# Kernel optimization log

Hardware: AMD Instinct MI355X
Metric: run time of the kernel (lower is better)

Reference implementation:

```python
import jax, jax.numpy as jnp
import numpy as np


def setup_inputs() -> dict:
    key = jax.random.key(0)
    k1, k2, k3, k4 = jax.random.split(key, 4)
    B, Tv, Ta, D = 8, 2048, 2048, 256
    return {
        "visual_features": jax.random.normal(k1, (B, Tv, D), dtype=jnp.float32),
        "audio_features": jax.random.normal(k2, (B, Ta, D), dtype=jnp.float32),
        "visual_weights": jax.random.uniform(k3, (D, D), dtype=jnp.float32),
        "audio_weights": jax.random.uniform(k4, (D, D), dtype=jnp.float32),
        "num_neighbors": 8,
    }


def _pairwise_l2(vm, am):
    # ||v - a|| via the expanded form to avoid the [B,Tv,Ta,D] intermediate.
    sq = (
        jnp.sum(vm * vm, -1)[:, :, None]
        + jnp.sum(am * am, -1)[:, None, :]
        - 2.0 * jnp.einsum("btd,bsd->bts", vm, am)
    )
    sq = jnp.maximum(sq, 0.0)
    # safe sqrt: subgradient 0 at 0 (matches torch.norm backward convention)
    return jnp.where(sq > 0, jnp.sqrt(jnp.where(sq > 0, sq, 1.0)), 0.0)


def reference(visual_features, audio_features, visual_weights, audio_weights, num_neighbors):
    vm = visual_features @ visual_weights  # [B,Tv,D]
    am = audio_features @ audio_weights    # [B,Ta,D]
    graph = jnp.exp(-_pairwise_l2(vm, am))  # [B,Tv,Ta]
    # topk over the visual axis (dim=1): move it last for lax.top_k
    _, idx = jax.lax.top_k(jnp.swapaxes(graph, 1, 2), num_neighbors)  # [B,Ta,k]
    idx = jnp.swapaxes(idx, 1, 2)  # [B,k,Ta]
    # broadcasted gather along axis 1: result [B,k,Ta,D]
    vn = jnp.take_along_axis(visual_features[:, :, None, :], idx[..., None], axis=1)
    an = jnp.take_along_axis(audio_features[:, :, None, :], idx[..., None], axis=1)
    # mean over dim=2 (the Ta axis of the gathered neighbors) -> [B,k,D]
    return vn.mean(axis=2), an.mean(axis=2)
```

## Files before the change

### kernel.cpp

```cpp
#include <hip/hip_runtime.h>
#include <cstddef>
#include <cstdint>

namespace {
constexpr int kB   = 8;
constexpr int kT   = 2048;
constexpr int kD   = 256;
constexpr int kK   = 8;
constexpr int kM   = kB * kT;
constexpr int kNC  = kB * kT;
constexpr int kColCap = 64;
constexpr int kOvCap  = 1 << 17;
constexpr int kStr = 264;
constexpr float kMinNormalF = 1.17549435e-38f;
}

typedef __attribute__((ext_vector_type(8)))  __bf16 bf16x8;
typedef __attribute__((ext_vector_type(16))) float  f32x16;

__device__ inline unsigned short f2bf_rne(float x) {
  unsigned u = __float_as_uint(x);
  unsigned r = (u + 0x7FFFu + ((u >> 16) & 1u)) >> 16;
  return (unsigned short)r;
}
__device__ inline float bf2f(unsigned short h) {
  return __uint_as_float((unsigned)h << 16);
}
union FragU { uint4 u4; bf16x8 v; };

__device__ inline void async16(const unsigned short* g, unsigned short* l) {
  __builtin_amdgcn_global_load_lds(
      (const __attribute__((address_space(1))) unsigned int*)(const void*)g,
      (__attribute__((address_space(3))) unsigned int*)(void*)l, 16, 0, 0);
}

__device__ inline void stage_tile_async(const unsigned short* src,
                                        unsigned short* S, int w, int lane) {
  const int hi = lane >> 5, lo = lane & 31;
#pragma unroll
  for (int i = 0; i < 8; ++i) {
    const int p = w * 8 + i;
    const int rowl = p * 2 + hi;
    const int c = lo ^ (rowl & 31);
    async16(src + (size_t)rowl * kD + c * 8, S + p * 512);
  }
}
__device__ inline uint4 lds_frag(const unsigned short* S, int row, int kc, int half) {
  const int c = (kc * 2 + half) ^ (row & 31);
  return *reinterpret_cast<const uint4*>(S + row * 256 + c * 8);
}

__global__ __launch_bounds__(256) void prep(const float* __restrict__ W0,
                                            const float* __restrict__ W1,
                                            unsigned short* __restrict__ T0,
                                            unsigned short* __restrict__ T1,
                                            unsigned* __restrict__ zeroBase,
                                            int zeroWords) {
  const int blk = blockIdx.x;
  if (blk < 128) {
    const float* W = (blk & 64) ? W1 : W0;
    unsigned short* WT = (blk & 64) ? T1 : T0;
    const int t = blk & 63;
    const int c0 = (t & 7) * 32, k0 = (t >> 3) * 32;
    __shared__ float tile[32][33];
    const int tx = threadIdx.x & 31, ty = threadIdx.x >> 5;
#pragma unroll
    for (int i = 0; i < 4; ++i)
      tile[ty + i * 8][tx] = W[(size_t)(k0 + ty + i * 8) * kD + c0 + tx];
    __syncthreads();
#pragma unroll
    for (int i = 0; i < 4; ++i)
      WT[(size_t)(c0 + ty + i * 8) * kD + k0 + tx] = f2bf_rne(tile[tx][ty + i * 8]);
  } else {
    for (int i = (blk - 128) * 256 + threadIdx.x; i < zeroWords; i += 32 * 256)
      zeroBase[i] = 0u;
  }
}

__global__ __launch_bounds__(256) void gemm_hyb(const float* __restrict__ Xv,
                                                const float* __restrict__ Xa,
                                                const unsigned short* __restrict__ WvT,
                                                const unsigned short* __restrict__ WaT,
                                                unsigned short* __restrict__ Cv,
                                                unsigned short* __restrict__ Ca,
                                                float* __restrict__ nv,
                                                float* __restrict__ na) {
  __shared__ unsigned short S[64 * kStr];
  const int z = blockIdx.z;
  const float* X = z ? Xa : Xv;
  const unsigned short* WT = z ? WaT : WvT;
  unsigned short* Cb = z ? Ca : Cv;
  float* nrm = z ? na : nv;
  const int r0 = blockIdx.x * 64;
  const int cHalf = blockIdx.y;
  const int tid = threadIdx.x;
  const int w = tid >> 6, lane = tid & 63;
  const int wt = w & 1, wc = w >> 1;
  const int half = lane >> 5, ln = lane & 31;

#pragma unroll
  for (int i = 0; i < 16; ++i) {
    const int idx = i * 256 + tid;
    const int row = idx >> 6, g = idx & 63;
    const float4 v = *reinterpret_cast<const float4*>(X + (size_t)(r0 + row) * kD + g * 4);
    ushort4 o;
    o.x = f2bf_rne(v.x); o.y = f2bf_rne(v.y); o.z = f2bf_rne(v.z); o.w = f2bf_rne(v.w);
    *reinterpret_cast<ushort4*>(S + row * kStr + g * 4) = o;
  }
  __syncthreads();
  uint4 afr[16];
#pragma unroll
  for (int kc = 0; kc < 16; ++kc)
    afr[kc] = *reinterpret_cast<const uint4*>(S + (wt * 32 + ln) * kStr + kc * 16 + half * 8);

  float ns[16];
#pragma unroll
  for (int r = 0; r < 16; ++r) ns[r] = 0.0f;

  for (int ct = 0; ct < 2; ++ct) {
    const int c0 = (cHalf * 2 + ct) * 64;
    __syncthreads();
    stage_tile_async(WT + (size_t)c0 * kD, S, w, lane);
    __syncthreads();
    f32x16 acc;
#pragma unroll
    for (int i = 0; i < 16; ++i) acc[i] = 0.0f;
#pragma unroll
    for (int kc = 0; kc < 16; ++kc) {
      FragU fa, fb;
      fa.u4 = afr[kc];
      fb.u4 = lds_frag(S, wc * 32 + ln, kc, half);
      acc = __builtin_amdgcn_mfma_f32_32x32x16_bf16(fa.v, fb.v, acc, 0, 0, 0);
    }
    const int col = c0 + wc * 32 + ln;
#pragma unroll
    for (int r = 0; r < 16; ++r) {
      const int row = r0 + wt * 32 + (r & 3) + 8 * (r >> 2) + 4 * half;
      const unsigned short us = f2bf_rne(acc[r]);
      Cb[(size_t)row * kD + col] = us;
      const float f = bf2f(us);
      ns[r] += f * f;
    }
  }
#pragma unroll
  for (int r = 0; r < 16; ++r) {
    float v = ns[r];
#pragma unroll
    for (int off = 1; off < 32; off <<= 1) v += __shfl_xor(v, off, 64);
    if (ln == 0) {
      const int row = r0 + wt * 32 + (r & 3) + 8 * (r >> 2) + 4 * half;
      atomicAdd(nrm + row, v);
    }
  }
}

__global__ __launch_bounds__(256) void keys_v14(const unsigned short* __restrict__ vmb,
                                                const unsigned short* __restrict__ amb,
                                                const float* __restrict__ vn2,
                                                const float* __restrict__ an2,
                                                unsigned* __restrict__ colCount,
                                                uint2* __restrict__ colRecs,
                                                unsigned* __restrict__ ovCount,
                                                uint2* __restrict__ ovRecs) {
  __shared__ unsigned short S[64 * 256];
  const int b = blockIdx.z;
  const int t0 = blockIdx.x * 128;
  const int sr0 = blockIdx.y * 256;
  const int tid = threadIdx.x;
  const int w = tid >> 6, lane = tid & 63;
  const int half = lane >> 5, ln = lane & 31;

  uint4 afr[16];
#pragma unroll
  for (int h = 0; h < 2; ++h) {
    __syncthreads();
    stage_tile_async(vmb + ((size_t)b * kT + t0 + h * 64) * kD, S, w, lane);
    __syncthreads();
    if ((w >> 1) == h) {
#pragma unroll
      for (int kc = 0; kc < 16; ++kc)
        afr[kc] = lds_frag(S, (w & 1) * 32 + ln, kc, half);
    }
  }

  const float* v2p = vn2 + (size_t)b * kT + t0 + w * 32;

  for (int st = 0; st < 4; ++st) {
    const int s0 = sr0 + st * 64;
    __syncthreads();
    stage_tile_async(amb + ((size_t)b * kT + s0) * kD, S, w, lane);
    __syncthreads();
    f32x16 acc[2];
#pragma unroll
    for (int j = 0; j < 2; ++j)
#pragma unroll
      for (int i = 0; i < 16; ++i) acc[j][i] = 0.0f;
#pragma unroll
    for (int kc = 0; kc < 16; ++kc) {
      FragU fa; fa.u4 = afr[kc];
#pragma unroll
      for (int ss = 0; ss < 2; ++ss) {
        FragU fb;
        fb.u4 = lds_frag(S, ss * 32 + ln, kc, half);
        acc[ss] = __builtin_amdgcn_mfma_f32_32x32x16_bf16(fa.v, fb.v, acc[ss], 0, 0, 0);
      }
    }
#pragma unroll
    for (int ss = 0; ss < 2; ++ss) {
      const int s = s0 + ss * 32 + ln;
      const float a2 = an2[(size_t)b * kT + s];
      const int c = (b << 11) | s;
#pragma unroll
      for (int g = 0; g < 4; ++g) {
        const float4 v2 = *reinterpret_cast<const float4*>(v2p + g * 8 + half * 4);
        const float v2a[4] = {v2.x, v2.y, v2.z, v2.w};
#pragma unroll
        for (int q = 0; q < 4; ++q) {
          const float raw = v2a[q] + a2 - 2.0f * acc[ss][4 * g + q];
          if (raw < 7744.0f) {
            const float dist = sqrtf(fmaxf(raw, 0.0f));
            const float e = expf(-dist);
            if (e >= kMinNormalF) {
              const int t = t0 + w * 32 + g * 8 + half * 4 + q;
              const unsigned slot = atomicAdd(&colCount[c], 1u);
              if (slot < (unsigned)kColCap) {
                colRecs[(size_t)c * kColCap + slot] = make_uint2(__float_as_uint(e), (unsigned)t);
              } else {
                const unsigned pos = ((unsigned)b << 22) | ((unsigned)s << 11) | (unsigned)t;
                const unsigned oi = atomicAdd(ovCount, 1u);
                if (oi < (unsigned)kOvCap) ovRecs[oi] = make_uint2(__float_as_uint(e), pos);
              }
            }
          }
        }
      }
    }
  }
}

__global__ __launch_bounds__(256) void gather_fused(const float* __restrict__ visual,
                                                    const float* __restrict__ audio,
                                                    const unsigned* __restrict__ colCount,
                                                    const uint2* __restrict__ colRecs,
                                                    const unsigned* __restrict__ ovCount,
                                                    const uint2* __restrict__ ovRecs,
                                                    float* __restrict__ pv,
                                                    float* __restrict__ pa) {
  __shared__ int sIdx[32];
  const int u = blockIdx.x;
  const int bj = u >> 6, ch = u & 63;
  const int b = bj >> 3, j = bj & 7;
  const int tid = threadIdx.x;
  if (tid < 32) {
    const int s = ch * 32 + tid;
    const int c = (b << 11) | s;
    unsigned K[8]; int T[8];
#pragma unroll
    for (int i = 0; i < 8; ++i) { K[i] = 0u; T[i] = 0x7FFFFFFF; }
    const int cnt = (int)colCount[c];
    const int m = min(cnt, kColCap);
    for (int i = 0; i < m; ++i) {
      const uint2 r = colRecs[(size_t)c * kColCap + i];
      const unsigned kx = r.x; const int tx = (int)r.y;
      if (kx > K[7] || (kx == K[7] && tx < T[7])) {
        K[7] = kx; T[7] = tx;
#pragma unroll
        for (int q = 7; q >= 1; --q) {
          const bool sw = (K[q] > K[q - 1]) || (K[q] == K[q - 1] && T[q] < T[q - 1]);
          if (sw) {
            const unsigned tk = K[q]; K[q] = K[q - 1]; K[q - 1] = tk;
            const int tt = T[q];      T[q] = T[q - 1]; T[q - 1] = tt;
          }
        }
      }
    }
    if (cnt > kColCap) {
      int n = (int)*ovCount;
      if (n > kOvCap) n = kOvCap;
      for (int i = 0; i < n; ++i) {
        const uint2 r = ovRecs[i];
        if ((int)(r.y >> 11) == c) {
          const unsigned kx = r.x; const int tx = (int)(r.y & 2047u);
          if (kx > K[7] || (kx == K[7] && tx < T[7])) {
            K[7] = kx; T[7] = tx;
#pragma unroll
            for (int q = 7; q >= 1; --q) {
              const bool sw = (K[q] > K[q - 1]) || (K[q] == K[q - 1] && T[q] < T[q - 1]);
              if (sw) {
                const unsigned tk = K[q]; K[q] = K[q - 1]; K[q - 1] = tk;
                const int tt = T[q];      T[q] = T[q - 1]; T[q - 1] = tt;
              }
            }
          }
        }
      }
    }
    int mcnt = 0;
#pragma unroll
    for (int i = 0; i < 8; ++i) if (K[i] > 0u) mcnt++;
    int outv[8];
#pragma unroll
    for (int i = 0; i < 8; ++i) outv[i] = T[i];
    int cand = 0;
    for (int r = mcnt; r < 8; ++r) {
      bool taken = true;
      while (taken) {
        taken = false;
#pragma unroll
        for (int q = 0; q < 8; ++q)
          if (q < mcnt && T[q] == cand) taken = true;
        if (taken) cand++;
      }
      outv[r] = cand++;
    }
    sIdx[tid] = outv[j];
  }
  __syncthreads();
  float accV = 0.f, accA = 0.f;
  for (int i = 0; i < 32; ++i) {
    const int t = sIdx[i];
    const size_t base = ((size_t)b * kT + t) * kD + tid;
    accV += visual[base];
    accA += audio[base];
  }
  pv[(size_t)u * kD + tid] = accV;
  pa[(size_t)u * kD + tid] = accA;
}

__global__ __launch_bounds__(256) void reduce_kernel(const float* __restrict__ pv,
                                                     const float* __restrict__ pa,
                                                     float* __restrict__ out) {
  const int bj = blockIdx.x;
  const int d = threadIdx.x;
  float sV = 0.f, sA = 0.f;
#pragma unroll 8
  for (int ch = 0; ch < 64; ++ch) {
    sV += pv[((size_t)bj * 64 + ch) * kD + d];
    sA += pa[((size_t)bj * 64 + ch) * kD + d];
  }
  out[(size_t)bj * kD + d] = sV * (1.0f / kT);
  out[(size_t)kB * kK * kD + (size_t)bj * kD + d] = sA * (1.0f / kT);
}

extern "C" void kernel_launch(void* const* d_in, const int* in_sizes, int n_in,
                              void* d_out, int out_size, void* d_ws, size_t ws_size,
                              hipStream_t stream) {
  (void)in_sizes; (void)n_in; (void)out_size; (void)ws_size;
  const float* visual = (const float*)d_in[0];
  const float* audio  = (const float*)d_in[1];
  const float* Wv     = (const float*)d_in[2];
  const float* Wa     = (const float*)d_in[3];
  float* out = (float*)d_out;

  char* ws = (char*)d_ws;
  unsigned short* WvT = (unsigned short*)ws;
  unsigned short* WaT = WvT + (size_t)kD * kD;
  unsigned short* vmb = WaT + (size_t)kD * kD;
  unsigned short* amb = vmb + (size_t)kM * kD;
  float* vn2 = (float*)(amb + (size_t)kM * kD);
  float* an2 = vn2 + kM;
  unsigned* colCount = (unsigned*)(an2 + kM);
  unsigned* ovCount  = colCount + kNC;
  uint2* colRecs = (uint2*)(ovCount + 8);
  uint2* ovRecs  = colRecs + (size_t)kNC * kColCap;
  float* pv = (float*)(ovRecs + kOvCap);
  float* pa = pv + (size_t)4096 * kD;
  const int zeroWords = 2 * kM + kNC + 8;

  prep<<<dim3(160), 256, 0, stream>>>(Wv, Wa, WvT, WaT, (unsigned*)vn2, zeroWords);
  gemm_hyb<<<dim3(kM / 64, 2, 2), 256, 0, stream>>>(visual, audio, WvT, WaT,
                                                    vmb, amb, vn2, an2);
  keys_v14<<<dim3(kT / 128, kT / 256, kB), 256, 0, stream>>>(vmb, amb, vn2, an2,
                                                             colCount, colRecs, ovCount, ovRecs);
  gather_fused<<<dim3(4096), 256, 0, stream>>>(visual, audio, colCount, colRecs,
                                               ovCount, ovRecs, pv, pa);
  reduce_kernel<<<dim3(kB * kK), 256, 0, stream>>>(pv, pa, out);
}
```

Measured before the change: 156.6 us.

## Fuse final reduction into gather via atomics and compute full GEMM row per block

Drops the separate reduce kernel: gather blocks atomically add their scaled partial sums straight into the output, which prep now zeroes. The projection GEMM covers all four column tiles per block instead of splitting columns across two blocks, so the fp32-to-bf16 staging of each input row block is not repeated. The keys kernel epilogue is reordered so each v2 float4 is loaded once and used for both s sub-tiles. In exchange the output accumulation order is nondeterministic, and the GEMM grid has half as many blocks.

```diff
diff --git a/kernel.cpp b/kernel.cpp
--- a/kernel.cpp
+++ b/kernel.cpp
@@ -55,7 +55,8 @@
                                             unsigned short* __restrict__ T0,
                                             unsigned short* __restrict__ T1,
                                             unsigned* __restrict__ zeroBase,
-                                            int zeroWords) {
+                                            int zeroWords,
+                                            unsigned* __restrict__ outW) {
   const int blk = blockIdx.x;
   if (blk < 128) {
     const float* W = (blk & 64) ? W1 : W0;
@@ -74,6 +75,8 @@
   } else {
     for (int i = (blk - 128) * 256 + threadIdx.x; i < zeroWords; i += 32 * 256)
       zeroBase[i] = 0u;
+    for (int i = (blk - 128) * 256 + threadIdx.x; i < 2 * kB * kK * kD; i += 32 * 256)
+      outW[i] = 0u;
   }
 }
 
@@ -92,7 +95,6 @@
   unsigned short* Cb = z ? Ca : Cv;
   float* nrm = z ? na : nv;
   const int r0 = blockIdx.x * 64;
-  const int cHalf = blockIdx.y;
   const int tid = threadIdx.x;
   const int w = tid >> 6, lane = tid & 63;
   const int wt = w & 1, wc = w >> 1;
@@ -117,8 +119,8 @@
 #pragma unroll
   for (int r = 0; r < 16; ++r) ns[r] = 0.0f;
 
-  for (int ct = 0; ct < 2; ++ct) {
-    const int c0 = (cHalf * 2 + ct) * 64;
+  for (int ct = 0; ct < 4; ++ct) {
+    const int c0 = ct * 64;
     __syncthreads();
     stage_tile_async(WT + (size_t)c0 * kD, S, w, lane);
     __syncthreads();
@@ -205,15 +207,19 @@
         acc[ss] = __builtin_amdgcn_mfma_f32_32x32x16_bf16(fa.v, fb.v, acc[ss], 0, 0, 0);
       }
     }
-#pragma unroll
-    for (int ss = 0; ss < 2; ++ss) {
-      const int s = s0 + ss * 32 + ln;
-      const float a2 = an2[(size_t)b * kT + s];
-      const int c = (b << 11) | s;
-#pragma unroll
-      for (int g = 0; g < 4; ++g) {
-        const float4 v2 = *reinterpret_cast<const float4*>(v2p + g * 8 + half * 4);
-        const float v2a[4] = {v2.x, v2.y, v2.z, v2.w};
+    float a2s[2];
+#pragma unroll
+    for (int ss = 0; ss < 2; ++ss)
+      a2s[ss] = an2[(size_t)b * kT + s0 + ss * 32 + ln];
+#pragma unroll
+    for (int g = 0; g < 4; ++g) {
+      const float4 v2 = *reinterpret_cast<const float4*>(v2p + g * 8 + half * 4);
+      const float v2a[4] = {v2.x, v2.y, v2.z, v2.w};
+#pragma unroll
+      for (int ss = 0; ss < 2; ++ss) {
+        const int s = s0 + ss * 32 + ln;
+        const float a2 = a2s[ss];
+        const int c = (b << 11) | s;
 #pragma unroll
         for (int q = 0; q < 4; ++q) {
           const float raw = v2a[q] + a2 - 2.0f * acc[ss][4 * g + q];
@@ -244,8 +250,7 @@
                                                     const uint2* __restrict__ colRecs,
                                                     const unsigned* __restrict__ ovCount,
                                                     const uint2* __restrict__ ovRecs,
-                                                    float* __restrict__ pv,
-                                                    float* __restrict__ pa) {
+                                                    float* __restrict__ out) {
   __shared__ int sIdx[32];
   const int u = blockIdx.x;
   const int bj = u >> 6, ch = u & 63;
@@ -323,23 +328,8 @@
     accV += visual[base];
     accA += audio[base];
   }
-  pv[(size_t)u * kD + tid] = accV;
-  pa[(size_t)u * kD + tid] = accA;
-}
-
-__global__ __launch_bounds__(256) void reduce_kernel(const float* __restrict__ pv,
-                                                     const float* __restrict__ pa,
-                                                     float* __restrict__ out) {
-  const int bj = blockIdx.x;
-  const int d = threadIdx.x;
-  float sV = 0.f, sA = 0.f;
-#pragma unroll 8
-  for (int ch = 0; ch < 64; ++ch) {
-    sV += pv[((size_t)bj * 64 + ch) * kD + d];
-    sA += pa[((size_t)bj * 64 + ch) * kD + d];
-  }
-  out[(size_t)bj * kD + d] = sV * (1.0f / kT);
-  out[(size_t)kB * kK * kD + (size_t)bj * kD + d] = sA * (1.0f / kT);
+  atomicAdd(&out[(size_t)bj * kD + tid], accV * (1.0f / kT));
+  atomicAdd(&out[(size_t)kB * kK * kD + (size_t)bj * kD + tid], accA * (1.0f / kT));
 }
 
 extern "C" void kernel_launch(void* const* d_in, const int* in_sizes, int n_in,
@@ -363,16 +353,14 @@
   unsigned* ovCount  = colCount + kNC;
   uint2* colRecs = (uint2*)(ovCount + 8);
   uint2* ovRecs  = colRecs + (size_t)kNC * kColCap;
-  float* pv = (float*)(ovRecs + kOvCap);
-  float* pa = pv + (size_t)4096 * kD;
   const int zeroWords = 2 * kM + kNC + 8;
 
-  prep<<<dim3(160), 256, 0, stream>>>(Wv, Wa, WvT, WaT, (unsigned*)vn2, zeroWords);
-  gemm_hyb<<<dim3(kM / 64, 2, 2), 256, 0, stream>>>(visual, audio, WvT, WaT,
+  prep<<<dim3(160), 256, 0, stream>>>(Wv, Wa, WvT, WaT, (unsigned*)vn2, zeroWords,
+                                      (unsigned*)out);
+  gemm_hyb<<<dim3(kM / 64, 1, 2), 256, 0, stream>>>(visual, audio, WvT, WaT,
                                                     vmb, amb, vn2, an2);
   keys_v14<<<dim3(kT / 128, kT / 256, kB), 256, 0, stream>>>(vmb, amb, vn2, an2,
                                                              colCount, colRecs, ovCount, ovRecs);
   gather_fused<<<dim3(4096), 256, 0, stream>>>(visual, audio, colCount, colRecs,
-                                               ovCount, ovRecs, pv, pa);
-  reduce_kernel<<<dim3(kB * kK), 256, 0, stream>>>(pv, pa, out);
-}
+                                               ovCount, ovRecs, out);
+}
```

After: 152.3 us. 1.03x faster.
